# Kernel tuning notes

Measured on AMD Instinct MI355X. Metric: run time of the kernel, lower is better.

## Reference

```python
import jax, jax.numpy as jnp
import numpy as np

D_IN, D_K, D_V = 768, 128, 768


def setup_inputs() -> dict:
    key = jax.random.key(0)
    ks = jax.random.split(key, 7)
    x = jax.random.normal(ks[0], (4, 2048, D_IN), dtype=jnp.float32)
    s_in = 1.0 / np.sqrt(D_IN)
    Wq = jax.random.uniform(ks[1], (D_IN, D_K), minval=-s_in, maxval=s_in, dtype=jnp.float32)
    bq = jax.random.uniform(ks[2], (D_K,), minval=-s_in, maxval=s_in, dtype=jnp.float32)
    Wk = jax.random.uniform(ks[3], (D_IN, D_K), minval=-s_in, maxval=s_in, dtype=jnp.float32)
    bk = jax.random.uniform(ks[4], (D_K,), minval=-s_in, maxval=s_in, dtype=jnp.float32)
    Wv = jax.random.uniform(ks[5], (D_IN, D_V), minval=-s_in, maxval=s_in, dtype=jnp.float32)
    bv = jax.random.uniform(ks[6], (D_V,), minval=-s_in, maxval=s_in, dtype=jnp.float32)
    return {"x": x, "Wq": Wq, "bq": bq, "Wk": Wk, "bk": bk, "Wv": Wv, "bv": bv}


def reference(x, Wq, bq, Wk, bk, Wv, bv):
    # q,k: [b,t,d_k]; v: [b,t,d_v]
    q = jnp.einsum('bti,ik->btk', x, Wq) + bq
    k = jnp.einsum('bti,ik->btk', x, Wk) + bk
    v = jnp.einsum('bti,iv->btv', x, Wv) + bv
    scale = 1.0 / jnp.sqrt(jnp.asarray(D_K, dtype=jnp.float32))
    scores = jnp.einsum('bqk,btk->bqt', q, k) * scale  # [b,t,t]
    attn = jax.nn.softmax(scores, axis=-1)
    return jnp.einsum('bqt,btv->bqv', attn, v)
```

## Files before the change

kernel.cpp:

```cpp
#include <hip/hip_runtime.h>
#include <stdint.h>

typedef unsigned short u16;
typedef __attribute__((ext_vector_type(8))) short short8;
typedef __attribute__((ext_vector_type(4))) float f32x4;

#define BATCH 4
#define SEQ   2048
#define DIN   768
#define DK    128
#define DV    768
#define MTOT  (BATCH*SEQ)
#define NQKV  1024

__device__ __forceinline__ u16 f2bf(float f) {
  union { float f; uint32_t u; } v; v.f = f;
  uint32_t r = v.u + 0x7FFFu + ((v.u >> 16) & 1u);
  return (u16)(r >> 16);
}

template<int N> __device__ __forceinline__ void wait_vmcnt() {
  if constexpr (N == 0) asm volatile("s_waitcnt vmcnt(0)" ::: "memory");
  else if constexpr (N == 5) asm volatile("s_waitcnt vmcnt(5)" ::: "memory");
  else if constexpr (N == 10) asm volatile("s_waitcnt vmcnt(10)" ::: "memory");
}

__global__ __launch_bounds__(256) void prep(
    const float* __restrict__ x, u16* __restrict__ xb,
    const float* __restrict__ Wq, const float* __restrict__ bq,
    const float* __restrict__ Wk, const float* __restrict__ bk,
    const float* __restrict__ Wv, const float* __restrict__ bv,
    u16* __restrict__ WbT, float* __restrict__ biasP) {
  const float qs = 0.088388347648318447f;
  __shared__ u16 tile[64][72];
  int b = blockIdx.x;
  int tid = threadIdx.x;
  if (b < 6144) {
    int i = (b * 256 + tid) * 4;
    float4 v = *(const float4*)(x + i);
    u16 o[4] = { f2bf(v.x), f2bf(v.y), f2bf(v.z), f2bf(v.w) };
    *(uint2*)(xb + i) = *(const uint2*)o;
    return;
  }
  int bid2 = b - 6144;
  int y   = bid2 / 12;
  int i0  = (bid2 - y * 12) * 64;
  const float* W; u16* dst; int ldw, nb; float sc;
  if (y < 2)      { W = Wq; dst = WbT;                      ldw = DK; sc = qs;   nb = y;     }
  else if (y < 4) { W = Wk; dst = WbT + (size_t)DK * DIN;   ldw = DK; sc = 1.0f; nb = y - 2; }
  else            { W = Wv; dst = WbT + (size_t)2*DK * DIN; ldw = DV; sc = 1.0f; nb = y - 4; }
  int n0 = nb * 64;
  if (i0 == 0 && y == 0) {
    for (int n = tid; n < NQKV; n += 256)
      biasP[n] = (n < DK) ? bq[n] * qs : (n < 2*DK ? bk[n - DK] : bv[n - 2*DK]);
  }
  int tr = tid >> 2;
  int tc = (tid & 3) * 16;
  const float* src = W + (size_t)(i0 + tr) * ldw + n0 + tc;
  u16 o[16];
#pragma unroll
  for (int u = 0; u < 16; u += 4) {
    float4 v = *(const float4*)(src + u);
    o[u] = f2bf(v.x * sc); o[u+1] = f2bf(v.y * sc); o[u+2] = f2bf(v.z * sc); o[u+3] = f2bf(v.w * sc);
  }
  *(uint4*)&tile[tr][tc]     = *(const uint4*)&o[0];
  *(uint4*)&tile[tr][tc + 8] = *(const uint4*)&o[8];
  __syncthreads();
  u16 tmp[16];
#pragma unroll
  for (int u = 0; u < 16; ++u) tmp[u] = tile[tc + u][tr];
  u16* d = dst + (size_t)(n0 + tr) * DIN + i0 + tc;
  *(uint4*)d       = *(const uint4*)&tmp[0];
  *(uint4*)(d + 8) = *(const uint4*)&tmp[8];
}

__global__ __launch_bounds__(512, 4) void gemm_proj(
    const u16* __restrict__ A, const u16* __restrict__ BT,
    u16* __restrict__ C0, u16* __restrict__ C1,
    const float* __restrict__ bias)
{
  const int NJ = 2, CH = 4, gx = 64;
  __shared__ u16 As[2][128][64];
  __shared__ u16 Bs[2][NJ * 64][64];
  const int tid = threadIdx.x;
  const int l   = tid & 63;
  const int wid = tid >> 6;
  const int wm  = wid >> 2;
  const int wn  = wid & 3;

  const int nwg = gridDim.x;
  const int cpx = nwg >> 3;
  const int bid = blockIdx.x;
  const int wg  = (bid & 7) * cpx + (bid >> 3);
  const int by  = wg / gx;
  const int bx  = wg - by * gx;
  const int m0  = bx * 128;
  const int n0  = by * (NJ * 64);

  f32x4 acc[4][NJ] = {};
  const int lr = l >> 3;
  const int lc = ((l & 7) ^ lr) * 8;
  const int ca = wid * CH;

  auto STAGE = [&](int buf, int k0) {
#pragma unroll
    for (int i = 0; i < CH; ++i) {
      int c = ca + i;
      if (c < 16) {
        const u16* src = A + (size_t)(m0 + c * 8 + lr) * DIN + k0 + lc;
        __builtin_amdgcn_global_load_lds(
            (const __attribute__((address_space(1))) unsigned int*)src,
            (__attribute__((address_space(3))) unsigned int*)&As[buf][c * 8][0],
            16, 0, 0);
      } else {
        int cb = c - 16;
        const u16* src = BT + (size_t)(n0 + cb * 8 + lr) * DIN + k0 + lc;
        __builtin_amdgcn_global_load_lds(
            (const __attribute__((address_space(1))) unsigned int*)src,
            (__attribute__((address_space(3))) unsigned int*)&Bs[buf][cb * 8][0],
            16, 0, 0);
      }
    }
  };

  STAGE(0, 0);
  __syncthreads();
  int cur = 0;
  for (int k0 = 0; k0 < DIN; k0 += 64) {
    if (k0 + 64 < DIN) STAGE(cur ^ 1, k0 + 64);
#pragma unroll
    for (int ks = 0; ks < 2; ++ks) {
      short8 af[4], bg[NJ];
#pragma unroll
      for (int i = 0; i < 4; ++i) {
        int row  = wm * 64 + i * 16 + (l & 15);
        int slot = (ks * 4 + (l >> 4)) ^ (row & 7);
        af[i] = *(const short8*)&As[cur][row][slot * 8];
      }
#pragma unroll
      for (int j = 0; j < NJ; ++j) {
        int row  = wn * (NJ * 16) + j * 16 + (l & 15);
        int slot = (ks * 4 + (l >> 4)) ^ (row & 7);
        bg[j] = *(const short8*)&Bs[cur][row][slot * 8];
      }
#pragma unroll
      for (int i = 0; i < 4; ++i)
#pragma unroll
        for (int j = 0; j < NJ; ++j)
          acc[i][j] = __builtin_amdgcn_mfma_f32_16x16x32_bf16(af[i], bg[j], acc[i][j], 0, 0, 0);
    }
    __syncthreads();
    cur ^= 1;
  }

  const int rbase = (l >> 4) * 4;
  const int cl    = l & 15;
#pragma unroll
  for (int i = 0; i < 4; ++i) {
#pragma unroll
    for (int j = 0; j < NJ; ++j) {
      int col = n0 + wn * (NJ * 16) + j * 16 + cl;
      int row0 = m0 + wm * 64 + i * 16 + rbase;
      float bv_ = bias[col];
      if (n0 < 256) {
#pragma unroll
        for (int q = 0; q < 4; ++q)
          C0[(size_t)(row0 + q) * 256 + col] = f2bf(acc[i][j][q] + bv_);
      } else {
        int b = row0 >> 11, t = row0 & 2047;
        u16 o[4];
#pragma unroll
        for (int q = 0; q < 4; ++q) o[q] = f2bf(acc[i][j][q] + bv_);
        *(uint2*)&C1[((size_t)b * DV + (col - 256)) * SEQ + t] = *(const uint2*)o;
      }
    }
  }
}

__global__ __launch_bounds__(512, 2) void gemm_pv(
    const u16* __restrict__ P, const u16* __restrict__ vT,
    float* __restrict__ out)
{
  const int NJ = 3, CH = 5, gx = 16, gy = 4, NT = SEQ / 64;
  __shared__ u16 As[3][128][64];
  __shared__ u16 Bs[3][NJ * 64][64];
  const int tid = threadIdx.x;
  const int l   = tid & 63;
  const int wid = tid >> 6;
  const int wm  = wid >> 2;
  const int wn  = wid & 3;

  const int nwg = gridDim.x;
  const int cpx = nwg >> 3;
  const int bid = blockIdx.x;
  const int wg  = (bid & 7) * cpx + (bid >> 3);
  const int z   = wg / (gx * gy);
  const int rem = wg - z * gx * gy;
  const int by  = rem / gx;
  const int bx  = rem - by * gx;
  const int m0  = bx * 128;
  const int n0  = by * (NJ * 64);

  const u16* A  = P  + (size_t)z * SEQ * SEQ;
  const u16* BT = vT + (size_t)z * DV * SEQ;

  f32x4 acc[4][NJ] = {};
  f32x4 accO[4] = {};
  const short8 kOnes = {16256,16256,16256,16256,16256,16256,16256,16256};

  const int lr = l >> 3;
  const int lc = ((l & 7) ^ lr) * 8;
  const int ca = wid * CH;

  auto STAGE = [&](int buf, int k0, int i0, int i1) {
#pragma unroll
    for (int i = 0; i < CH; ++i) {
      if (i < i0 || i >= i1) continue;
      int c = ca + i;
      if (c < 16) {
        const u16* src = A + (size_t)(m0 + c * 8 + lr) * SEQ + k0 + lc;
        __builtin_amdgcn_global_load_lds(
            (const __attribute__((address_space(1))) unsigned int*)src,
            (__attribute__((address_space(3))) unsigned int*)&As[buf][c * 8][0],
            16, 0, 0);
      } else {
        int cb = c - 16;
        const u16* src = BT + (size_t)(n0 + cb * 8 + lr) * SEQ + k0 + lc;
        __builtin_amdgcn_global_load_lds(
            (const __attribute__((address_space(1))) unsigned int*)src,
            (__attribute__((address_space(3))) unsigned int*)&Bs[buf][cb * 8][0],
            16, 0, 0);
      }
    }
  };

  STAGE(0, 0, 0, CH);
  STAGE(1, 64, 0, CH);
  int cur = 0;
  for (int t = 0; t < NT; ++t) {
    if (t == NT - 1) wait_vmcnt<0>(); else wait_vmcnt<CH>();
    __builtin_amdgcn_s_barrier();
    const int nxt2 = (cur + 2 >= 3) ? cur - 1 : cur + 2;
    const bool pf = (t + 2 < NT);
#pragma unroll
    for (int ks = 0; ks < 2; ++ks) {
      short8 af[4], bg[NJ];
#pragma unroll
      for (int i = 0; i < 4; ++i) {
        int row  = wm * 64 + i * 16 + (l & 15);
        int slot = (ks * 4 + (l >> 4)) ^ (row & 7);
        af[i] = *(const short8*)&As[cur][row][slot * 8];
      }
#pragma unroll
      for (int j = 0; j < NJ; ++j) {
        int row  = wn * (NJ * 16) + j * 16 + (l & 15);
        int slot = (ks * 4 + (l >> 4)) ^ (row & 7);
        bg[j] = *(const short8*)&Bs[cur][row][slot * 8];
      }
      if (pf) {
        if (ks == 0) STAGE(nxt2, (t + 2) * 64, 0, 3);
        else         STAGE(nxt2, (t + 2) * 64, 3, CH);
      }
      __builtin_amdgcn_s_setprio(1);
#pragma unroll
      for (int i = 0; i < 4; ++i) {
#pragma unroll
        for (int j = 0; j < NJ; ++j)
          acc[i][j] = __builtin_amdgcn_mfma_f32_16x16x32_bf16(af[i], bg[j], acc[i][j], 0, 0, 0);
        accO[i] = __builtin_amdgcn_mfma_f32_16x16x32_bf16(af[i], kOnes, accO[i], 0, 0, 0);
      }
      __builtin_amdgcn_s_setprio(0);
    }
    cur = (cur + 1 == 3) ? 0 : cur + 1;
  }

  const int rbase = (l >> 4) * 4;
  const int cl    = l & 15;
#pragma unroll
  for (int i = 0; i < 4; ++i) {
    f32x4 rs;
#pragma unroll
    for (int q = 0; q < 4; ++q) rs[q] = 1.0f / accO[i][q];
#pragma unroll
    for (int j = 0; j < NJ; ++j) {
      int col  = n0 + wn * (NJ * 16) + j * 16 + cl;
      int row0 = m0 + wm * 64 + i * 16 + rbase;
#pragma unroll
      for (int q = 0; q < 4; ++q)
        out[(size_t)z * SEQ * DV + (size_t)(row0 + q) * DV + col] = acc[i][j][q] * rs[q];
    }
  }
}

__global__ __launch_bounds__(512, 4) void sgemm_exp(
    const u16* __restrict__ qk, u16* __restrict__ P)
{
  __shared__ u16 As[128][128];
  __shared__ u16 Bs[128][128];
  const int tid = threadIdx.x;
  const int l   = tid & 63;
  const int wid = tid >> 6;
  const int wm  = wid >> 2;
  const int wn  = wid & 3;

  const int nwg = gridDim.x;
  const int cpx = nwg >> 3;
  const int bid = blockIdx.x;
  const int wg  = (bid & 7) * cpx + (bid >> 3);
  const int z   = wg >> 8;
  const int rem = wg & 255;
  const int by  = rem >> 4;
  const int bx  = rem & 15;
  const int m0  = bx * 128;
  const int n0  = by * 128;

  const u16* A  = qk + (size_t)z * SEQ * 256;
  const u16* BT = qk + DK + (size_t)z * SEQ * 256;

  const int rin  = l >> 4;
  const int s16  = l & 15;
#pragma unroll
  for (int i = 0; i < 8; ++i) {
    int c = wid * 8 + i;
    if (c < 32) {
      int r = c * 4 + rin;
      int gs = s16 ^ (r & 7);
      const u16* src = A + (size_t)(m0 + r) * 256 + gs * 8;
      __builtin_amdgcn_global_load_lds(
          (const __attribute__((address_space(1))) unsigned int*)src,
          (__attribute__((address_space(3))) unsigned int*)&As[c * 4][0],
          16, 0, 0);
    } else {
      int cb = c - 32;
      int r = cb * 4 + rin;
      int gs = s16 ^ (r & 7);
      const u16* src = BT + (size_t)(n0 + r) * 256 + gs * 8;
      __builtin_amdgcn_global_load_lds(
          (const __attribute__((address_space(1))) unsigned int*)src,
          (__attribute__((address_space(3))) unsigned int*)&Bs[cb * 4][0],
          16, 0, 0);
    }
  }
  __syncthreads();

  f32x4 acc[4][2] = {};
#pragma unroll
  for (int ks = 0; ks < 4; ++ks) {
    short8 af[4], bg[2];
#pragma unroll
    for (int i = 0; i < 4; ++i) {
      int row  = wm * 64 + i * 16 + (l & 15);
      int slot = (ks * 4 + (l >> 4)) ^ (row & 7);
      af[i] = *(const short8*)&As[row][slot * 8];
    }
#pragma unroll
    for (int j = 0; j < 2; ++j) {
      int row  = wn * 32 + j * 16 + (l & 15);
      int slot = (ks * 4 + (l >> 4)) ^ (row & 7);
      bg[j] = *(const short8*)&Bs[row][slot * 8];
    }
#pragma unroll
    for (int i = 0; i < 4; ++i)
#pragma unroll
      for (int j = 0; j < 2; ++j)
        acc[i][j] = __builtin_amdgcn_mfma_f32_16x16x32_bf16(af[i], bg[j], acc[i][j], 0, 0, 0);
  }

  const int rbase = (l >> 4) * 4;
  const int cl    = l & 15;
  u16* Pz = P + (size_t)z * SEQ * SEQ;
#pragma unroll
  for (int i = 0; i < 4; ++i)
#pragma unroll
    for (int j = 0; j < 2; ++j) {
      int col  = n0 + wn * 32 + j * 16 + cl;
      int row0 = m0 + wm * 64 + i * 16 + rbase;
#pragma unroll
      for (int q = 0; q < 4; ++q)
        Pz[(size_t)(row0 + q) * SEQ + col] = f2bf(__expf(acc[i][j][q]));
    }
}

extern "C" void kernel_launch(void* const* d_in, const int* in_sizes, int n_in,
                              void* d_out, int out_size, void* d_ws, size_t ws_size,
                              hipStream_t stream) {
  const float* x  = (const float*)d_in[0];
  const float* Wq = (const float*)d_in[1];
  const float* bq = (const float*)d_in[2];
  const float* Wk = (const float*)d_in[3];
  const float* bk = (const float*)d_in[4];
  const float* Wv = (const float*)d_in[5];
  const float* bv = (const float*)d_in[6];
  float* out = (float*)d_out;

  size_t off = 0;
  auto alloc = [&](size_t bytes) -> void* {
    void* p = (char*)d_ws + off;
    off += (bytes + 255) & ~(size_t)255;
    return p;
  };
  u16*   xb    = (u16*)alloc((size_t)MTOT * DIN * 2);
  u16*   WbT   = (u16*)alloc((size_t)NQKV * DIN * 2);
  float* biasP = (float*)alloc(NQKV * 4);
  u16*   qk    = (u16*)alloc((size_t)MTOT * 256 * 2);
  u16*   vT    = (u16*)alloc((size_t)BATCH * DV * SEQ * 2);
  u16*   P     = (u16*)alloc((size_t)BATCH * SEQ * SEQ * 2);
  if (off > ws_size) return;

  prep<<<dim3(6144 + 192), dim3(256), 0, stream>>>(x, xb, Wq, bq, Wk, bk, Wv, bv, WbT, biasP);

  gemm_proj<<<dim3(64 * 8), dim3(512), 0, stream>>>(xb, WbT, qk, vT, biasP);

  sgemm_exp<<<dim3(16 * 16 * BATCH), dim3(512), 0, stream>>>(qk, P);

  gemm_pv<<<dim3(16 * 4 * BATCH), dim3(512), 0, stream>>>(P, vT, out);
}
```

Baseline: 84.45 us.

## Compute softmax row sums via atomics in score kernel instead of ones-MFMA

```diff
diff --git a/kernel.cpp b/kernel.cpp
--- a/kernel.cpp
+++ b/kernel.cpp
@@ -18,6 +18,10 @@
   uint32_t r = v.u + 0x7FFFu + ((v.u >> 16) & 1u);
   return (u16)(r >> 16);
 }
+__device__ __forceinline__ float bf2f(u16 h) {
+  union { uint32_t u; float f; } v; v.u = ((uint32_t)h) << 16;
+  return v.f;
+}
 
 template<int N> __device__ __forceinline__ void wait_vmcnt() {
   if constexpr (N == 0) asm volatile("s_waitcnt vmcnt(0)" ::: "memory");
@@ -30,7 +34,7 @@
     const float* __restrict__ Wq, const float* __restrict__ bq,
     const float* __restrict__ Wk, const float* __restrict__ bk,
     const float* __restrict__ Wv, const float* __restrict__ bv,
-    u16* __restrict__ WbT, float* __restrict__ biasP) {
+    u16* __restrict__ WbT, float* __restrict__ biasP, float* __restrict__ rsum) {
   const float qs = 0.088388347648318447f;
   __shared__ u16 tile[64][72];
   int b = blockIdx.x;
@@ -40,6 +44,11 @@
     float4 v = *(const float4*)(x + i);
     u16 o[4] = { f2bf(v.x), f2bf(v.y), f2bf(v.z), f2bf(v.w) };
     *(uint2*)(xb + i) = *(const uint2*)o;
+    return;
+  }
+  if (b >= 6144 + 192) {
+    int i = (b - 6144 - 192) * 1024 + tid * 4;
+    *(float4*)(rsum + i) = make_float4(0.f, 0.f, 0.f, 0.f);
     return;
   }
   int bid2 = b - 6144;
@@ -177,123 +186,8 @@
   }
 }
 
-__global__ __launch_bounds__(512, 2) void gemm_pv(
-    const u16* __restrict__ P, const u16* __restrict__ vT,
-    float* __restrict__ out)
-{
-  const int NJ = 3, CH = 5, gx = 16, gy = 4, NT = SEQ / 64;
-  __shared__ u16 As[3][128][64];
-  __shared__ u16 Bs[3][NJ * 64][64];
-  const int tid = threadIdx.x;
-  const int l   = tid & 63;
-  const int wid = tid >> 6;
-  const int wm  = wid >> 2;
-  const int wn  = wid & 3;
-
-  const int nwg = gridDim.x;
-  const int cpx = nwg >> 3;
-  const int bid = blockIdx.x;
-  const int wg  = (bid & 7) * cpx + (bid >> 3);
-  const int z   = wg / (gx * gy);
-  const int rem = wg - z * gx * gy;
-  const int by  = rem / gx;
-  const int bx  = rem - by * gx;
-  const int m0  = bx * 128;
-  const int n0  = by * (NJ * 64);
-
-  const u16* A  = P  + (size_t)z * SEQ * SEQ;
-  const u16* BT = vT + (size_t)z * DV * SEQ;
-
-  f32x4 acc[4][NJ] = {};
-  f32x4 accO[4] = {};
-  const short8 kOnes = {16256,16256,16256,16256,16256,16256,16256,16256};
-
-  const int lr = l >> 3;
-  const int lc = ((l & 7) ^ lr) * 8;
-  const int ca = wid * CH;
-
-  auto STAGE = [&](int buf, int k0, int i0, int i1) {
-#pragma unroll
-    for (int i = 0; i < CH; ++i) {
-      if (i < i0 || i >= i1) continue;
-      int c = ca + i;
-      if (c < 16) {
-        const u16* src = A + (size_t)(m0 + c * 8 + lr) * SEQ + k0 + lc;
-        __builtin_amdgcn_global_load_lds(
-            (const __attribute__((address_space(1))) unsigned int*)src,
-            (__attribute__((address_space(3))) unsigned int*)&As[buf][c * 8][0],
-            16, 0, 0);
-      } else {
-        int cb = c - 16;
-        const u16* src = BT + (size_t)(n0 + cb * 8 + lr) * SEQ + k0 + lc;
-        __builtin_amdgcn_global_load_lds(
-            (const __attribute__((address_space(1))) unsigned int*)src,
-            (__attribute__((address_space(3))) unsigned int*)&Bs[buf][cb * 8][0],
-            16, 0, 0);
-      }
-    }
-  };
-
-  STAGE(0, 0, 0, CH);
-  STAGE(1, 64, 0, CH);
-  int cur = 0;
-  for (int t = 0; t < NT; ++t) {
-    if (t == NT - 1) wait_vmcnt<0>(); else wait_vmcnt<CH>();
-    __builtin_amdgcn_s_barrier();
-    const int nxt2 = (cur + 2 >= 3) ? cur - 1 : cur + 2;
-    const bool pf = (t + 2 < NT);
-#pragma unroll
-    for (int ks = 0; ks < 2; ++ks) {
-      short8 af[4], bg[NJ];
-#pragma unroll
-      for (int i = 0; i < 4; ++i) {
-        int row  = wm * 64 + i * 16 + (l & 15);
-        int slot = (ks * 4 + (l >> 4)) ^ (row & 7);
-        af[i] = *(const short8*)&As[cur][row][slot * 8];
-      }
-#pragma unroll
-      for (int j = 0; j < NJ; ++j) {
-        int row  = wn * (NJ * 16) + j * 16 + (l & 15);
-        int slot = (ks * 4 + (l >> 4)) ^ (row & 7);
-        bg[j] = *(const short8*)&Bs[cur][row][slot * 8];
-      }
-      if (pf) {
-        if (ks == 0) STAGE(nxt2, (t + 2) * 64, 0, 3);
-        else         STAGE(nxt2, (t + 2) * 64, 3, CH);
-      }
-      __builtin_amdgcn_s_setprio(1);
-#pragma unroll
-      for (int i = 0; i < 4; ++i) {
-#pragma unroll
-        for (int j = 0; j < NJ; ++j)
-          acc[i][j] = __builtin_amdgcn_mfma_f32_16x16x32_bf16(af[i], bg[j], acc[i][j], 0, 0, 0);
-        accO[i] = __builtin_amdgcn_mfma_f32_16x16x32_bf16(af[i], kOnes, accO[i], 0, 0, 0);
-      }
-      __builtin_amdgcn_s_setprio(0);
-    }
-    cur = (cur + 1 == 3) ? 0 : cur + 1;
-  }
-
-  const int rbase = (l >> 4) * 4;
-  const int cl    = l & 15;
-#pragma unroll
-  for (int i = 0; i < 4; ++i) {
-    f32x4 rs;
-#pragma unroll
-    for (int q = 0; q < 4; ++q) rs[q] = 1.0f / accO[i][q];
-#pragma unroll
-    for (int j = 0; j < NJ; ++j) {
-      int col  = n0 + wn * (NJ * 16) + j * 16 + cl;
-      int row0 = m0 + wm * 64 + i * 16 + rbase;
-#pragma unroll
-      for (int q = 0; q < 4; ++q)
-        out[(size_t)z * SEQ * DV + (size_t)(row0 + q) * DV + col] = acc[i][j][q] * rs[q];
-    }
-  }
-}
-
 __global__ __launch_bounds__(512, 4) void sgemm_exp(
-    const u16* __restrict__ qk, u16* __restrict__ P)
+    const u16* __restrict__ qk, u16* __restrict__ P, float* __restrict__ rsum)
 {
   __shared__ u16 As[128][128];
   __shared__ u16 Bs[128][128];
@@ -369,6 +263,7 @@
   const int rbase = (l >> 4) * 4;
   const int cl    = l & 15;
   u16* Pz = P + (size_t)z * SEQ * SEQ;
+  float ex[4][2][4];
 #pragma unroll
   for (int i = 0; i < 4; ++i)
 #pragma unroll
@@ -376,9 +271,136 @@
       int col  = n0 + wn * 32 + j * 16 + cl;
       int row0 = m0 + wm * 64 + i * 16 + rbase;
 #pragma unroll
+      for (int q = 0; q < 4; ++q) {
+        u16 h = f2bf(__expf(acc[i][j][q]));
+        ex[i][j][q] = bf2f(h);
+        Pz[(size_t)(row0 + q) * SEQ + col] = h;
+      }
+    }
+  float* rs_g = rsum + (size_t)z * SEQ;
+#pragma unroll
+  for (int i = 0; i < 4; ++i)
+#pragma unroll
+    for (int q = 0; q < 4; ++q) {
+      float s = ex[i][0][q] + ex[i][1][q];
+      s += __shfl_xor(s, 1, 64);
+      s += __shfl_xor(s, 2, 64);
+      s += __shfl_xor(s, 4, 64);
+      s += __shfl_xor(s, 8, 64);
+      if (cl == 0) atomicAdd(&rs_g[m0 + wm * 64 + i * 16 + rbase + q], s);
+    }
+}
+
+__global__ __launch_bounds__(512, 2) void gemm_pv(
+    const u16* __restrict__ P, const u16* __restrict__ vT,
+    const float* __restrict__ rsum, float* __restrict__ out)
+{
+  const int NJ = 3, CH = 5, gx = 16, gy = 4, NT = SEQ / 64;
+  __shared__ u16 As[3][128][64];
+  __shared__ u16 Bs[3][NJ * 64][64];
+  const int tid = threadIdx.x;
+  const int l   = tid & 63;
+  const int wid = tid >> 6;
+  const int wm  = wid >> 2;
+  const int wn  = wid & 3;
+
+  const int nwg = gridDim.x;
+  const int cpx = nwg >> 3;
+  const int bid = blockIdx.x;
+  const int wg  = (bid & 7) * cpx + (bid >> 3);
+  const int z   = wg / (gx * gy);
+  const int rem = wg - z * gx * gy;
+  const int by  = rem / gx;
+  const int bx  = rem - by * gx;
+  const int m0  = bx * 128;
+  const int n0  = by * (NJ * 64);
+
+  const u16* A  = P  + (size_t)z * SEQ * SEQ;
+  const u16* BT = vT + (size_t)z * DV * SEQ;
+
+  f32x4 acc[4][NJ] = {};
+
+  const int lr = l >> 3;
+  const int lc = ((l & 7) ^ lr) * 8;
+  const int ca = wid * CH;
+
+  auto STAGE = [&](int buf, int k0, int i0, int i1) {
+#pragma unroll
+    for (int i = 0; i < CH; ++i) {
+      if (i < i0 || i >= i1) continue;
+      int c = ca + i;
+      if (c < 16) {
+        const u16* src = A + (size_t)(m0 + c * 8 + lr) * SEQ + k0 + lc;
+        __builtin_amdgcn_global_load_lds(
+            (const __attribute__((address_space(1))) unsigned int*)src,
+            (__attribute__((address_space(3))) unsigned int*)&As[buf][c * 8][0],
+            16, 0, 0);
+      } else {
+        int cb = c - 16;
+        const u16* src = BT + (size_t)(n0 + cb * 8 + lr) * SEQ + k0 + lc;
+        __builtin_amdgcn_global_load_lds(
+            (const __attribute__((address_space(1))) unsigned int*)src,
+            (__attribute__((address_space(3))) unsigned int*)&Bs[buf][cb * 8][0],
+            16, 0, 0);
+      }
+    }
+  };
+
+  STAGE(0, 0, 0, CH);
+  STAGE(1, 64, 0, CH);
+  int cur = 0;
+  for (int t = 0; t < NT; ++t) {
+    if (t == NT - 1) wait_vmcnt<0>(); else wait_vmcnt<CH>();
+    __builtin_amdgcn_s_barrier();
+    const int nxt2 = (cur + 2 >= 3) ? cur - 1 : cur + 2;
+    const bool pf = (t + 2 < NT);
+#pragma unroll
+    for (int ks = 0; ks < 2; ++ks) {
+      short8 af[4], bg[NJ];
+#pragma unroll
+      for (int i = 0; i < 4; ++i) {
+        int row  = wm * 64 + i * 16 + (l & 15);
+        int slot = (ks * 4 + (l >> 4)) ^ (row & 7);
+        af[i] = *(const short8*)&As[cur][row][slot * 8];
+      }
+#pragma unroll
+      for (int j = 0; j < NJ; ++j) {
+        int row  = wn * (NJ * 16) + j * 16 + (l & 15);
+        int slot = (ks * 4 + (l >> 4)) ^ (row & 7);
+        bg[j] = *(const short8*)&Bs[cur][row][slot * 8];
+      }
+      if (pf) {
+        if (ks == 0) STAGE(nxt2, (t + 2) * 64, 0, 3);
+        else         STAGE(nxt2, (t + 2) * 64, 3, CH);
+      }
+      __builtin_amdgcn_s_setprio(1);
+#pragma unroll
+      for (int i = 0; i < 4; ++i)
+#pragma unroll
+        for (int j = 0; j < NJ; ++j)
+          acc[i][j] = __builtin_amdgcn_mfma_f32_16x16x32_bf16(af[i], bg[j], acc[i][j], 0, 0, 0);
+      __builtin_amdgcn_s_setprio(0);
+    }
+    cur = (cur + 1 == 3) ? 0 : cur + 1;
+  }
+
+  const int rbase = (l >> 4) * 4;
+  const int cl    = l & 15;
+  const float* rs_g = rsum + (size_t)z * SEQ;
+#pragma unroll
+  for (int i = 0; i < 4; ++i) {
+    int row0 = m0 + wm * 64 + i * 16 + rbase;
+    float4 rv = *(const float4*)&rs_g[row0];
+    f32x4 rs;
+    rs[0] = 1.0f / rv.x; rs[1] = 1.0f / rv.y; rs[2] = 1.0f / rv.z; rs[3] = 1.0f / rv.w;
+#pragma unroll
+    for (int j = 0; j < NJ; ++j) {
+      int col = n0 + wn * (NJ * 16) + j * 16 + cl;
+#pragma unroll
       for (int q = 0; q < 4; ++q)
-        Pz[(size_t)(row0 + q) * SEQ + col] = f2bf(__expf(acc[i][j][q]));
-    }
+        out[(size_t)z * SEQ * DV + (size_t)(row0 + q) * DV + col] = acc[i][j][q] * rs[q];
+    }
+  }
 }
 
 extern "C" void kernel_launch(void* const* d_in, const int* in_sizes, int n_in,
@@ -405,13 +427,14 @@
   u16*   qk    = (u16*)alloc((size_t)MTOT * 256 * 2);
   u16*   vT    = (u16*)alloc((size_t)BATCH * DV * SEQ * 2);
   u16*   P     = (u16*)alloc((size_t)BATCH * SEQ * SEQ * 2);
+  float* rsum  = (float*)alloc((size_t)MTOT * 4);
   if (off > ws_size) return;
 
-  prep<<<dim3(6144 + 192), dim3(256), 0, stream>>>(x, xb, Wq, bq, Wk, bk, Wv, bv, WbT, biasP);
+  prep<<<dim3(6144 + 192 + 8), dim3(256), 0, stream>>>(x, xb, Wq, bq, Wk, bk, Wv, bv, WbT, biasP, rsum);
 
   gemm_proj<<<dim3(64 * 8), dim3(512), 0, stream>>>(xb, WbT, qk, vT, biasP);
 
-  sgemm_exp<<<dim3(16 * 16 * BATCH), dim3(512), 0, stream>>>(qk, P);
-
-  gemm_pv<<<dim3(16 * 4 * BATCH), dim3(512), 0, stream>>>(P, vT, out);
-}
+  sgemm_exp<<<dim3(16 * 16 * BATCH), dim3(512), 0, stream>>>(qk, P, rsum);
+
+  gemm_pv<<<dim3(16 * 4 * BATCH), dim3(512), 0, stream>>>(P, vT, rsum, out);
+}
```

New measurement: 90.94 us. +7.7%, slower.

## Enlarge PV GEMM tile to 256x192 with double-buffered staging

Applied to the files above, without the earlier changes.

```diff
diff --git a/kernel.cpp b/kernel.cpp
--- a/kernel.cpp
+++ b/kernel.cpp
@@ -19,11 +19,10 @@
   return (u16)(r >> 16);
 }
 
-template<int N> __device__ __forceinline__ void wait_vmcnt() {
-  if constexpr (N == 0) asm volatile("s_waitcnt vmcnt(0)" ::: "memory");
-  else if constexpr (N == 5) asm volatile("s_waitcnt vmcnt(5)" ::: "memory");
-  else if constexpr (N == 10) asm volatile("s_waitcnt vmcnt(10)" ::: "memory");
-}
+#define GLOAD_LDS(SRC, DST) \
+  __builtin_amdgcn_global_load_lds( \
+      (const __attribute__((address_space(1))) unsigned int*)(SRC), \
+      (__attribute__((address_space(3))) unsigned int*)(DST), 16, 0, 0)
 
 __global__ __launch_bounds__(256) void prep(
     const float* __restrict__ x, u16* __restrict__ xb,
@@ -107,18 +106,10 @@
     for (int i = 0; i < CH; ++i) {
       int c = ca + i;
       if (c < 16) {
-        const u16* src = A + (size_t)(m0 + c * 8 + lr) * DIN + k0 + lc;
-        __builtin_amdgcn_global_load_lds(
-            (const __attribute__((address_space(1))) unsigned int*)src,
-            (__attribute__((address_space(3))) unsigned int*)&As[buf][c * 8][0],
-            16, 0, 0);
+        GLOAD_LDS(A + (size_t)(m0 + c * 8 + lr) * DIN + k0 + lc, &As[buf][c * 8][0]);
       } else {
         int cb = c - 16;
-        const u16* src = BT + (size_t)(n0 + cb * 8 + lr) * DIN + k0 + lc;
-        __builtin_amdgcn_global_load_lds(
-            (const __attribute__((address_space(1))) unsigned int*)src,
-            (__attribute__((address_space(3))) unsigned int*)&Bs[buf][cb * 8][0],
-            16, 0, 0);
+        GLOAD_LDS(BT + (size_t)(n0 + cb * 8 + lr) * DIN + k0 + lc, &Bs[buf][cb * 8][0]);
       }
     }
   };
@@ -173,121 +164,6 @@
         for (int q = 0; q < 4; ++q) o[q] = f2bf(acc[i][j][q] + bv_);
         *(uint2*)&C1[((size_t)b * DV + (col - 256)) * SEQ + t] = *(const uint2*)o;
       }
-    }
-  }
-}
-
-__global__ __launch_bounds__(512, 2) void gemm_pv(
-    const u16* __restrict__ P, const u16* __restrict__ vT,
-    float* __restrict__ out)
-{
-  const int NJ = 3, CH = 5, gx = 16, gy = 4, NT = SEQ / 64;
-  __shared__ u16 As[3][128][64];
-  __shared__ u16 Bs[3][NJ * 64][64];
-  const int tid = threadIdx.x;
-  const int l   = tid & 63;
-  const int wid = tid >> 6;
-  const int wm  = wid >> 2;
-  const int wn  = wid & 3;
-
-  const int nwg = gridDim.x;
-  const int cpx = nwg >> 3;
-  const int bid = blockIdx.x;
-  const int wg  = (bid & 7) * cpx + (bid >> 3);
-  const int z   = wg / (gx * gy);
-  const int rem = wg - z * gx * gy;
-  const int by  = rem / gx;
-  const int bx  = rem - by * gx;
-  const int m0  = bx * 128;
-  const int n0  = by * (NJ * 64);
-
-  const u16* A  = P  + (size_t)z * SEQ * SEQ;
-  const u16* BT = vT + (size_t)z * DV * SEQ;
-
-  f32x4 acc[4][NJ] = {};
-  f32x4 accO[4] = {};
-  const short8 kOnes = {16256,16256,16256,16256,16256,16256,16256,16256};
-
-  const int lr = l >> 3;
-  const int lc = ((l & 7) ^ lr) * 8;
-  const int ca = wid * CH;
-
-  auto STAGE = [&](int buf, int k0, int i0, int i1) {
-#pragma unroll
-    for (int i = 0; i < CH; ++i) {
-      if (i < i0 || i >= i1) continue;
-      int c = ca + i;
-      if (c < 16) {
-        const u16* src = A + (size_t)(m0 + c * 8 + lr) * SEQ + k0 + lc;
-        __builtin_amdgcn_global_load_lds(
-            (const __attribute__((address_space(1))) unsigned int*)src,
-            (__attribute__((address_space(3))) unsigned int*)&As[buf][c * 8][0],
-            16, 0, 0);
-      } else {
-        int cb = c - 16;
-        const u16* src = BT + (size_t)(n0 + cb * 8 + lr) * SEQ + k0 + lc;
-        __builtin_amdgcn_global_load_lds(
-            (const __attribute__((address_space(1))) unsigned int*)src,
-            (__attribute__((address_space(3))) unsigned int*)&Bs[buf][cb * 8][0],
-            16, 0, 0);
-      }
-    }
-  };
-
-  STAGE(0, 0, 0, CH);
-  STAGE(1, 64, 0, CH);
-  int cur = 0;
-  for (int t = 0; t < NT; ++t) {
-    if (t == NT - 1) wait_vmcnt<0>(); else wait_vmcnt<CH>();
-    __builtin_amdgcn_s_barrier();
-    const int nxt2 = (cur + 2 >= 3) ? cur - 1 : cur + 2;
-    const bool pf = (t + 2 < NT);
-#pragma unroll
-    for (int ks = 0; ks < 2; ++ks) {
-      short8 af[4], bg[NJ];
-#pragma unroll
-      for (int i = 0; i < 4; ++i) {
-        int row  = wm * 64 + i * 16 + (l & 15);
-        int slot = (ks * 4 + (l >> 4)) ^ (row & 7);
-        af[i] = *(const short8*)&As[cur][row][slot * 8];
-      }
-#pragma unroll
-      for (int j = 0; j < NJ; ++j) {
-        int row  = wn * (NJ * 16) + j * 16 + (l & 15);
-        int slot = (ks * 4 + (l >> 4)) ^ (row & 7);
-        bg[j] = *(const short8*)&Bs[cur][row][slot * 8];
-      }
-      if (pf) {
-        if (ks == 0) STAGE(nxt2, (t + 2) * 64, 0, 3);
-        else         STAGE(nxt2, (t + 2) * 64, 3, CH);
-      }
-      __builtin_amdgcn_s_setprio(1);
-#pragma unroll
-      for (int i = 0; i < 4; ++i) {
-#pragma unroll
-        for (int j = 0; j < NJ; ++j)
-          acc[i][j] = __builtin_amdgcn_mfma_f32_16x16x32_bf16(af[i], bg[j], acc[i][j], 0, 0, 0);
-        accO[i] = __builtin_amdgcn_mfma_f32_16x16x32_bf16(af[i], kOnes, accO[i], 0, 0, 0);
-      }
-      __builtin_amdgcn_s_setprio(0);
-    }
-    cur = (cur + 1 == 3) ? 0 : cur + 1;
-  }
-
-  const int rbase = (l >> 4) * 4;
-  const int cl    = l & 15;
-#pragma unroll
-  for (int i = 0; i < 4; ++i) {
-    f32x4 rs;
-#pragma unroll
-    for (int q = 0; q < 4; ++q) rs[q] = 1.0f / accO[i][q];
-#pragma unroll
-    for (int j = 0; j < NJ; ++j) {
-      int col  = n0 + wn * (NJ * 16) + j * 16 + cl;
-      int row0 = m0 + wm * 64 + i * 16 + rbase;
-#pragma unroll
-      for (int q = 0; q < 4; ++q)
-        out[(size_t)z * SEQ * DV + (size_t)(row0 + q) * DV + col] = acc[i][j][q] * rs[q];
     }
   }
 }
@@ -325,20 +201,12 @@
     if (c < 32) {
       int r = c * 4 + rin;
       int gs = s16 ^ (r & 7);
-      const u16* src = A + (size_t)(m0 + r) * 256 + gs * 8;
-      __builtin_amdgcn_global_load_lds(
-          (const __attribute__((address_space(1))) unsigned int*)src,
-          (__attribute__((address_space(3))) unsigned int*)&As[c * 4][0],
-          16, 0, 0);
+      GLOAD_LDS(A + (size_t)(m0 + r) * 256 + gs * 8, &As[c * 4][0]);
     } else {
       int cb = c - 32;
       int r = cb * 4 + rin;
       int gs = s16 ^ (r & 7);
-      const u16* src = BT + (size_t)(n0 + r) * 256 + gs * 8;
-      __builtin_amdgcn_global_load_lds(
-          (const __attribute__((address_space(1))) unsigned int*)src,
-          (__attribute__((address_space(3))) unsigned int*)&Bs[cb * 4][0],
-          16, 0, 0);
+      GLOAD_LDS(BT + (size_t)(n0 + r) * 256 + gs * 8, &Bs[cb * 4][0]);
     }
   }
   __syncthreads();
@@ -379,6 +247,106 @@
       for (int q = 0; q < 4; ++q)
         Pz[(size_t)(row0 + q) * SEQ + col] = f2bf(__expf(acc[i][j][q]));
     }
+}
+
+__global__ __launch_bounds__(512, 2) void gemm_pv(
+    const u16* __restrict__ P, const u16* __restrict__ vT,
+    float* __restrict__ out)
+{
+  const int NT = SEQ / 64;
+  __shared__ u16 As[2][256][64];
+  __shared__ u16 Bs[2][192][64];
+  const int tid = threadIdx.x;
+  const int l   = tid & 63;
+  const int wid = tid >> 6;
+  const int wm  = wid >> 1;
+  const int wn  = wid & 1;
+
+  const int nwg = gridDim.x;
+  const int cpx = nwg >> 3;
+  const int bid = blockIdx.x;
+  const int wg  = (bid & 7) * cpx + (bid >> 3);
+  const int z   = wg >> 5;
+  const int rem = wg & 31;
+  const int by  = rem >> 3;
+  const int bx  = rem & 7;
+  const int m0  = bx * 256;
+  const int nv0 = by * 192;
+
+  const u16* A  = P  + (size_t)z * SEQ * SEQ;
+  const u16* BT = vT + (size_t)z * DV * SEQ;
+
+  f32x4 acc[4][6] = {};
+  f32x4 accO[4] = {};
+  const short8 kOnes = {16256,16256,16256,16256,16256,16256,16256,16256};
+
+  const int lr = l >> 3;
+  const int lc = ((l & 7) ^ lr) * 8;
+  const int ca = wid * 7;
+
+  auto STAGE = [&](int buf, int k0) {
+#pragma unroll
+    for (int i = 0; i < 7; ++i) {
+      int c = ca + i;
+      if (c < 32) {
+        GLOAD_LDS(A + (size_t)(m0 + c * 8 + lr) * SEQ + k0 + lc, &As[buf][c * 8][0]);
+      } else {
+        int cb = c - 32;
+        GLOAD_LDS(BT + (size_t)(nv0 + cb * 8 + lr) * SEQ + k0 + lc, &Bs[buf][cb * 8][0]);
+      }
+    }
+  };
+
+  STAGE(0, 0);
+  __syncthreads();
+  int cur = 0;
+  for (int t = 0; t < NT; ++t) {
+    if (t + 1 < NT) STAGE(cur ^ 1, (t + 1) * 64);
+#pragma unroll
+    for (int ks = 0; ks < 2; ++ks) {
+      short8 af[4], bg[6];
+#pragma unroll
+      for (int i = 0; i < 4; ++i) {
+        int row  = wm * 64 + i * 16 + (l & 15);
+        int slot = (ks * 4 + (l >> 4)) ^ (row & 7);
+        af[i] = *(const short8*)&As[cur][row][slot * 8];
+      }
+#pragma unroll
+      for (int j = 0; j < 6; ++j) {
+        int row  = wn * 96 + j * 16 + (l & 15);
+        int slot = (ks * 4 + (l >> 4)) ^ (row & 7);
+        bg[j] = *(const short8*)&Bs[cur][row][slot * 8];
+      }
+      __builtin_amdgcn_s_setprio(1);
+#pragma unroll
+      for (int i = 0; i < 4; ++i) {
+#pragma unroll
+        for (int j = 0; j < 6; ++j)
+          acc[i][j] = __builtin_amdgcn_mfma_f32_16x16x32_bf16(af[i], bg[j], acc[i][j], 0, 0, 0);
+        accO[i] = __builtin_amdgcn_mfma_f32_16x16x32_bf16(af[i], kOnes, accO[i], 0, 0, 0);
+      }
+      __builtin_amdgcn_s_setprio(0);
+    }
+    __syncthreads();
+    cur ^= 1;
+  }
+
+  const int rbase = (l >> 4) * 4;
+  const int cl    = l & 15;
+#pragma unroll
+  for (int i = 0; i < 4; ++i) {
+    int row0 = m0 + wm * 64 + i * 16 + rbase;
+    f32x4 rs;
+#pragma unroll
+    for (int q = 0; q < 4; ++q) rs[q] = 1.0f / accO[i][q];
+#pragma unroll
+    for (int j = 0; j < 6; ++j) {
+      int col = nv0 + wn * 96 + j * 16 + cl;
+#pragma unroll
+      for (int q = 0; q < 4; ++q)
+        out[(size_t)z * SEQ * DV + (size_t)(row0 + q) * DV + col] = acc[i][j][q] * rs[q];
+    }
+  }
 }
 
 extern "C" void kernel_launch(void* const* d_in, const int* in_sizes, int n_in,
@@ -413,5 +381,5 @@
 
   sgemm_exp<<<dim3(16 * 16 * BATCH), dim3(512), 0, stream>>>(qk, P);
 
-  gemm_pv<<<dim3(16 * 4 * BATCH), dim3(512), 0, stream>>>(P, vT, out);
-}
+  gemm_pv<<<dim3(8 * 4 * BATCH), dim3(512), 0, stream>>>(P, vT, out);
+}
```

Result: slower. 109.9 us (+30.1%).
